# Performance work log

Hardware: AMD Instinct MI355X
Metric: run time of the kernel (lower is better)

The kernel has to match this reference:

```python
import jax, jax.numpy as jnp
import numpy as np

B, S, HID, NH, NS = 2, 1024, 2048, 16, 8
D = HID // NH  # head_dim = 128


def setup_inputs() -> dict:
    key = jax.random.key(0)
    ks = jax.random.split(key, 8)
    inv = 1.0 / np.sqrt(HID)
    return {
        "hidden_states": jax.random.normal(ks[0], (B, S, HID), jnp.float32),
        "Wq": jax.random.normal(ks[1], (HID, HID), jnp.float32) * inv,
        "Wk": jax.random.normal(ks[2], (HID, HID), jnp.float32) * inv,
        "Wv": jax.random.normal(ks[3], (HID, HID), jnp.float32) * inv,
        "Wo": jax.random.normal(ks[4], (HID, HID), jnp.float32) * inv,
        "splat_positions": jax.random.normal(ks[5], (NH, NS, D), jnp.float32) * 0.02,
        "splat_directions": jax.random.normal(ks[6], (NH, NS, D), jnp.float32) * 0.02,
        "splat_log_scales": jnp.full((NH, NS), np.log(0.8), jnp.float32),
        "splat_log_amplitudes": jnp.full((NH, NS), -np.log(float(NS)), jnp.float32),
        "directional_strength": jnp.float32(0.3),
        "gsa_strength": jnp.float32(-6.0),
    }


def _affinities(tokens, positions, directions, scales, dir_strength):
    # tokens [B,NH,S,D]; positions/directions [NH,NS,D]; scales [NH,NS]
    tok_sq = jnp.sum(tokens * tokens, axis=-1)                       # [B,NH,S]
    pos_sq = jnp.sum(positions * positions, axis=-1)                 # [NH,NS]
    tp = jnp.einsum('bhsd,hnd->bhsn', tokens, positions)             # [B,NH,S,NS]
    dist2 = tok_sq[..., None] - 2.0 * tp + pos_sq[None, :, None, :]
    dist2 = jnp.maximum(dist2, 0.0)
    # signed projection of (token - position) onto unit direction
    proj = (jnp.einsum('bhsd,hnd->bhsn', tokens, directions)
            - jnp.sum(positions * directions, axis=-1)[None, :, None, :])
    perp2 = jnp.maximum(dist2 - proj * proj, 0.0)
    inv2s2 = (0.5 / (scales * scales))[None, :, None, :]
    radial = jnp.exp(-dist2 * inv2s2)
    directional = jnp.exp(-perp2 * inv2s2)
    return (1.0 - dir_strength) * radial + dir_strength * directional


def reference(hidden_states, Wq, Wk, Wv, Wo, splat_positions, splat_directions,
              splat_log_scales, splat_log_amplitudes, directional_strength, gsa_strength):
    b, s, hid = hidden_states.shape

    def heads(x):  # [B,S,HID] -> [B,NH,S,D]
        return x.reshape(b, s, NH, D).transpose(0, 2, 1, 3)

    q = heads(hidden_states @ Wq)
    k = heads(hidden_states @ Wk)
    v = heads(hidden_states @ Wv)

    # --- standard (original) attention path ---
    scores = jnp.einsum('bhqd,bhkd->bhqk', q, k) / jnp.sqrt(jnp.float32(D))
    attn = jax.nn.softmax(scores, axis=-1)
    std = jnp.einsum('bhqk,bhkd->bhqd', attn, v)
    std = std.transpose(0, 2, 1, 3).reshape(b, s, hid) @ Wo

    # --- directional GSA path ---
    eps = 1e-12
    positions = splat_positions / (jnp.linalg.norm(splat_positions, axis=-1, keepdims=True) + eps)
    positions = positions * (np.sqrt(D) * 0.3)
    directions = splat_directions / (jnp.linalg.norm(splat_directions, axis=-1, keepdims=True) + eps)
    scales = jnp.clip(jnp.exp(splat_log_scales), 0.3, 1.2)
    amplitudes = jax.nn.softmax(splat_log_amplitudes, axis=-1)
    ds = jax.nn.sigmoid(directional_strength)

    qa = _affinities(q, positions, directions, scales, ds)  # [B,NH,S,NS]
    ka = _affinities(k, positions, directions, scales, ds)  # [B,NH,S,NS]
    w = jnp.einsum('bhqn,hn,bhkn->bhqk', qa, amplitudes, ka)
    w = w / (jnp.sum(w, axis=-1, keepdims=True) + 1e-8)
    dgsa = jnp.einsum('bhqk,bhkd->bhqd', w, v)
    dgsa = dgsa.transpose(0, 2, 1, 3).reshape(b, s, hid) @ Wo

    gsa = jax.nn.sigmoid(gsa_strength)
    blend = jnp.minimum(0.05, gsa * 0.1)
    return (1.0 - blend) * std + blend * dgsa
```

## Files before the change

### kernel.cpp

```cpp
#include <hip/hip_runtime.h>
#include <math.h>

typedef __attribute__((ext_vector_type(8))) short bf16x8;
typedef __attribute__((ext_vector_type(4))) float f32x4;
typedef unsigned short ushort_t;

__device__ __forceinline__ unsigned short f2b(float f) {
    unsigned u = __float_as_uint(f);
    unsigned r = (u + 0x7fffu + ((u >> 16) & 1u)) >> 16;
    return (unsigned short)r;
}
__device__ __forceinline__ float b2f(unsigned short h) {
    return __uint_as_float(((unsigned)h) << 16);
}

__device__ __forceinline__ void async_copy16(const void* g, void* l) {
    __builtin_amdgcn_global_load_lds((const __attribute__((address_space(1))) void*)g,
                                     (__attribute__((address_space(3))) void*)l, 16, 0, 0);
}

__global__ void splat_prep(const float* __restrict__ sp, const float* __restrict__ sd,
                           const float* __restrict__ ls, const float* __restrict__ la,
                           float* __restrict__ posn, float* __restrict__ dirn,
                           float* __restrict__ pos_sq, float* __restrict__ pdv,
                           float* __restrict__ iv2s2, float* __restrict__ amp) {
    int i = threadIdx.x;
    const float* p = sp + (size_t)i * 128;
    const float* d = sd + (size_t)i * 128;
    float np_ = 0.f, nd_ = 0.f;
    for (int k = 0; k < 128; ++k) { np_ += p[k] * p[k]; nd_ += d[k] * d[k]; }
    np_ = sqrtf(np_); nd_ = sqrtf(nd_);
    const float sc = 3.394112549695428f;
    float rp = sc / (np_ + 1e-12f);
    float rd = 1.f / (nd_ + 1e-12f);
    float psq = 0.f, pd_ = 0.f;
    for (int k = 0; k < 128; ++k) {
        float pn = p[k] * rp;
        float dn = d[k] * rd;
        posn[(size_t)i * 128 + k] = pn;
        dirn[(size_t)i * 128 + k] = dn;
        psq += pn * pn;
        pd_ += pn * dn;
    }
    pos_sq[i] = psq;
    pdv[i] = pd_;
    float s = expf(ls[i]);
    s = fminf(fmaxf(s, 0.3f), 1.2f);
    iv2s2[i] = 0.5f / (s * s);
    if ((i & 7) == 0) {
        int h = i >> 3;
        float mx = -INFINITY;
        for (int n = 0; n < 8; ++n) mx = fmaxf(mx, la[h * 8 + n]);
        float e[8]; float ssum = 0.f;
        for (int n = 0; n < 8; ++n) { e[n] = expf(la[h * 8 + n] - mx); ssum += e[n]; }
        for (int n = 0; n < 8; ++n) amp[h * 8 + n] = e[n] / ssum;
    }
}

__global__ __launch_bounds__(256) void convert_x(const float* __restrict__ X,
                                                 ushort_t* __restrict__ Y) {
    int i = (blockIdx.x * 256 + threadIdx.x) * 4;
    float4 v = *(const float4*)(X + i);
    ushort4 o;
    o.x = f2b(v.x); o.y = f2b(v.y); o.z = f2b(v.z); o.w = f2b(v.w);
    *(ushort4*)(Y + i) = o;
}

__global__ __launch_bounds__(256) void transpose_all(const float* __restrict__ W0,
                                                     const float* __restrict__ W1,
                                                     const float* __restrict__ W2,
                                                     const float* __restrict__ W3,
                                                     ushort_t* __restrict__ WT4) {
    __shared__ float t[32][33];
    int z = blockIdx.z;
    const float* W = (z == 0) ? W0 : (z == 1) ? W1 : (z == 2) ? W2 : W3;
    ushort_t* WT = WT4 + (size_t)z * 4194304;
    int tx = threadIdx.x & 31, ty = threadIdx.x >> 5;
    int bn = blockIdx.x * 32, bk = blockIdx.y * 32;
#pragma unroll
    for (int i = 0; i < 4; ++i)
        t[ty + i * 8][tx] = W[(size_t)(bk + ty + i * 8) * 2048 + bn + tx];
    __syncthreads();
#pragma unroll
    for (int i = 0; i < 4; ++i)
        WT[(size_t)(bn + ty + i * 8) * 2048 + bk + tx] = f2b(t[tx][ty + i * 8]);
}


__global__ __launch_bounds__(256) void gemm_qkv(const ushort_t* __restrict__ A,
                                                const ushort_t* __restrict__ WT4,
                                                ushort_t* __restrict__ Qb,
                                                ushort_t* __restrict__ Kb,
                                                ushort_t* __restrict__ Vb,
                                                ushort_t* __restrict__ Vt) {
    __shared__ ushort_t As[128 * 32];
    __shared__ ushort_t Bs[128 * 32];
    const int tid = threadIdx.x, lane = tid & 63, wave = tid >> 6;
    const int l15 = lane & 15, quad = lane >> 4;
    const int wm = (wave >> 1) * 64, wn = (wave & 1) * 64;
    const int bm = blockIdx.x * 128;
    const int by = blockIdx.y, which = by >> 4, bn = (by & 15) * 128;
    const ushort_t* BT = WT4 + (size_t)which * 4194304;
    f32x4 acc[4][4] = {};
    const int off0 = tid * 16;
    const int row0 = tid >> 2;
    const int c0 = (tid & 3) ^ ((row0 + (row0 >> 2)) & 3);
    const ushort_t* ga = A + (size_t)(bm + row0) * 2048 + c0 * 8;
    const ushort_t* gb = BT + (size_t)(bn + row0) * 2048 + c0 * 8;
    const int rsw = (l15 + (l15 >> 2)) & 3;
    for (int k0 = 0; k0 < 2048; k0 += 32) {
        __syncthreads();
        async_copy16(ga + k0, (char*)As + off0);
        async_copy16(ga + (size_t)64 * 2048 + k0, (char*)As + off0 + 4096);
        async_copy16(gb + k0, (char*)Bs + off0);
        async_copy16(gb + (size_t)64 * 2048 + k0, (char*)Bs + off0 + 4096);
        __syncthreads();
        bf16x8 af[4], bfr[4];
#pragma unroll
        for (int i = 0; i < 4; ++i)
            af[i] = *(const bf16x8*)((const char*)As + (wm + i * 16 + l15) * 64 + ((quad ^ rsw) << 4));
#pragma unroll
        for (int j = 0; j < 4; ++j)
            bfr[j] = *(const bf16x8*)((const char*)Bs + (wn + j * 16 + l15) * 64 + ((quad ^ rsw) << 4));
#pragma unroll
        for (int i = 0; i < 4; ++i)
#pragma unroll
            for (int j = 0; j < 4; ++j)
                acc[i][j] = __builtin_amdgcn_mfma_f32_16x16x32_bf16(af[i], bfr[j], acc[i][j], 0, 0, 0);
    }
    ushort_t* Cb = (which == 0) ? Qb : ((which == 1) ? Kb : Vb);
    const bool dot = (which == 2);
    const float oscale = (which == 0) ? 0.08838834764831845f : 1.f;
#pragma unroll
    for (int i = 0; i < 4; ++i) {
#pragma unroll
        for (int j = 0; j < 4; ++j) {
            int m0 = bm + wm + i * 16 + quad * 4;
            int n = bn + wn + j * 16 + l15;
            int b = m0 >> 10, s0 = m0 & 1023, h = n >> 7, d = n & 127;
            ushort4 pack;
            unsigned short* pp = (unsigned short*)&pack;
#pragma unroll
            for (int r = 0; r < 4; ++r) {
                unsigned short bv = f2b(acc[i][j][r] * oscale);
                pp[r] = bv;
                Cb[((size_t)((b << 4) | h) * 1024 + (s0 + r)) * 128 + d] = bv;
            }
            if (dot) *(ushort4*)(Vt + ((size_t)((b << 4) | h) * 128 + d) * 1024 + s0) = pack;
        }
    }
}

__global__ __launch_bounds__(256) void gemm_out(const ushort_t* __restrict__ A,
                                                const ushort_t* __restrict__ BT,
                                                float* __restrict__ Cf) {
    __shared__ ushort_t As[128 * 32];
    __shared__ ushort_t Bs[64 * 32];
    const int tid = threadIdx.x, lane = tid & 63, wave = tid >> 6;
    const int l15 = lane & 15, quad = lane >> 4;
    const int wm = (wave >> 1) * 64, wn = (wave & 1) * 32;
    const int bm = blockIdx.x * 128, bn = blockIdx.y * 64;
    f32x4 acc[4][2] = {};
    const int off0 = tid * 16;
    const int row0 = tid >> 2;
    const int c0 = (tid & 3) ^ ((row0 + (row0 >> 2)) & 3);
    const ushort_t* ga = A + (size_t)(bm + row0) * 2048 + c0 * 8;
    const ushort_t* gb = BT + (size_t)(bn + row0) * 2048 + c0 * 8;
    const int rsw = (l15 + (l15 >> 2)) & 3;
    for (int k0 = 0; k0 < 2048; k0 += 32) {
        __syncthreads();
        async_copy16(ga + k0, (char*)As + off0);
        async_copy16(ga + (size_t)64 * 2048 + k0, (char*)As + off0 + 4096);
        async_copy16(gb + k0, (char*)Bs + off0);
        __syncthreads();
        bf16x8 af[4], bfr[2];
#pragma unroll
        for (int i = 0; i < 4; ++i)
            af[i] = *(const bf16x8*)((const char*)As + (wm + i * 16 + l15) * 64 + ((quad ^ rsw) << 4));
#pragma unroll
        for (int j = 0; j < 2; ++j)
            bfr[j] = *(const bf16x8*)((const char*)Bs + (wn + j * 16 + l15) * 64 + ((quad ^ rsw) << 4));
#pragma unroll
        for (int i = 0; i < 4; ++i)
#pragma unroll
            for (int j = 0; j < 2; ++j)
                acc[i][j] = __builtin_amdgcn_mfma_f32_16x16x32_bf16(af[i], bfr[j], acc[i][j], 0, 0, 0);
    }
#pragma unroll
    for (int i = 0; i < 4; ++i)
#pragma unroll
        for (int j = 0; j < 2; ++j)
#pragma unroll
            for (int r = 0; r < 4; ++r) {
                int m = bm + wm + i * 16 + quad * 4 + r;
                int n = bn + wn + j * 16 + l15;
                Cf[(size_t)m * 2048 + n] = acc[i][j][r];
            }
}

__global__ __launch_bounds__(256) void affinity_kernel(
    const ushort_t* __restrict__ Q, const ushort_t* __restrict__ K,
    const float* __restrict__ posn, const float* __restrict__ dirn,
    const float* __restrict__ pos_sq, const float* __restrict__ pdv,
    const float* __restrict__ iv2s2, const float* __restrict__ ds_in,
    float* __restrict__ qa, float* __restrict__ ka) {
    int gid = blockIdx.x * 256 + threadIdx.x;
    int n = gid & 7;
    int t = (gid >> 3) & 32767;
    int which = gid >> 18;
    const ushort_t* T = (which ? K : Q) + (size_t)t * 128;
    int h = (t >> 10) & 15;
    const float* P = posn + (size_t)(h * 8 + n) * 128;
    const float* Dr = dirn + (size_t)(h * 8 + n) * 128;
    float tsq = 0.f, tp = 0.f, td = 0.f;
#pragma unroll
    for (int d = 0; d < 128; d += 8) {
        uint4 raw = *(const uint4*)(T + d);
        float tv[8];
        tv[0] = __uint_as_float(raw.x << 16); tv[1] = __uint_as_float(raw.x & 0xffff0000u);
        tv[2] = __uint_as_float(raw.y << 16); tv[3] = __uint_as_float(raw.y & 0xffff0000u);
        tv[4] = __uint_as_float(raw.z << 16); tv[5] = __uint_as_float(raw.z & 0xffff0000u);
        tv[6] = __uint_as_float(raw.w << 16); tv[7] = __uint_as_float(raw.w & 0xffff0000u);
        float4 p0 = *(const float4*)(P + d), p1 = *(const float4*)(P + d + 4);
        float4 d0 = *(const float4*)(Dr + d), d1 = *(const float4*)(Dr + d + 4);
        tsq += tv[0]*tv[0]+tv[1]*tv[1]+tv[2]*tv[2]+tv[3]*tv[3]+tv[4]*tv[4]+tv[5]*tv[5]+tv[6]*tv[6]+tv[7]*tv[7];
        tp  += tv[0]*p0.x+tv[1]*p0.y+tv[2]*p0.z+tv[3]*p0.w+tv[4]*p1.x+tv[5]*p1.y+tv[6]*p1.z+tv[7]*p1.w;
        td  += tv[0]*d0.x+tv[1]*d0.y+tv[2]*d0.z+tv[3]*d0.w+tv[4]*d1.x+tv[5]*d1.y+tv[6]*d1.z+tv[7]*d1.w;
    }
    float fs = which ? 1.f : 11.313708498984761f;
    tsq *= fs * fs; tp *= fs; td *= fs;
    float dist2 = fmaxf(tsq - 2.f * tp + pos_sq[h * 8 + n], 0.f);
    float proj = td - pdv[h * 8 + n];
    float perp2 = fmaxf(dist2 - proj * proj, 0.f);
    float iv = iv2s2[h * 8 + n];
    float dsv = 1.f / (1.f + __expf(-ds_in[0]));
    float aff = (1.f - dsv) * __expf(-dist2 * iv) + dsv * __expf(-perp2 * iv);
    (which ? ka : qa)[(size_t)t * 8 + n] = aff;
}

__global__ __launch_bounds__(128) void kv_s1_part(const float* __restrict__ ka,
                                                  const ushort_t* __restrict__ V,
                                                  float* __restrict__ KVp,
                                                  float* __restrict__ S1p) {
    int bh = blockIdx.x, sc = blockIdx.y;
    int d = threadIdx.x;
    const float* kaB = ka + ((size_t)bh * 1024 + sc * 128) * 8;
    const ushort_t* VB = V + ((size_t)bh * 1024 + sc * 128) * 128;
    float acc[8] = {};
#pragma unroll 4
    for (int s = 0; s < 128; ++s) {
        float vd = b2f(VB[(size_t)s * 128 + d]);
        float4 k0 = *(const float4*)(kaB + (size_t)s * 8);
        float4 k1 = *(const float4*)(kaB + (size_t)s * 8 + 4);
        acc[0] += k0.x * vd; acc[1] += k0.y * vd; acc[2] += k0.z * vd; acc[3] += k0.w * vd;
        acc[4] += k1.x * vd; acc[5] += k1.y * vd; acc[6] += k1.z * vd; acc[7] += k1.w * vd;
    }
#pragma unroll
    for (int n = 0; n < 8; ++n) KVp[(((size_t)bh * 8 + n) * 8 + sc) * 128 + d] = acc[n];
    __shared__ float s1p[128];
    {
        int n = d >> 4, chunk = d & 15;
        float p = 0.f;
        for (int s = chunk * 8; s < chunk * 8 + 8; ++s) p += kaB[(size_t)s * 8 + n];
        s1p[d] = p;
    }
    __syncthreads();
    if (d < 8) {
        float t = 0.f;
        for (int c = 0; c < 16; ++c) t += s1p[(d << 4) + c];
        S1p[((size_t)bh * 8 + d) * 8 + sc] = t;
    }
}

__global__ __launch_bounds__(256) void flash_blend(
    const ushort_t* __restrict__ Qg, const ushort_t* __restrict__ Kg,
    const ushort_t* __restrict__ Vtg,
    const float* __restrict__ qa, const float* __restrict__ amp,
    const float* __restrict__ S1p, const float* __restrict__ KVp,
    const float* __restrict__ gstr, ushort_t* __restrict__ blended) {
    __shared__ ushort_t Ks[2][64 * 128];
    __shared__ ushort_t Vt[2][128 * 64];
    __shared__ ushort_t Ps[4][16 * 72];
    __shared__ float KVs[8 * 128];
    __shared__ float S1s[8];
    const int tid = threadIdx.x, lane = tid & 63, wave = tid >> 6;
    const int l15 = lane & 15, quad = lane >> 4;
    const int bh = blockIdx.y, qt = blockIdx.x;

    const ushort_t* Qrow = Qg + ((size_t)(bh * 1024 + qt * 64 + wave * 16 + l15)) * 128 + quad * 8;
    bf16x8 aq[4];
#pragma unroll
    for (int k4 = 0; k4 < 4; ++k4) aq[k4] = *(const bf16x8*)(Qrow + k4 * 32);

    {
        int n = tid >> 5, d = (tid & 31) * 4;
        f32x4 kv = {};
#pragma unroll
        for (int sc = 0; sc < 8; ++sc)
            kv += *(const f32x4*)(KVp + (((size_t)bh * 8 + n) * 8 + sc) * 128 + d);
        *(f32x4*)(KVs + tid * 4) = kv;
    }
    if (tid < 8) {
        float s = 0.f;
#pragma unroll
        for (int sc = 0; sc < 8; ++sc) s += S1p[((size_t)bh * 8 + tid) * 8 + sc];
        S1s[tid] = s;
    }

    const ushort_t* Kbase = Kg + (size_t)bh * 131072;
    const ushort_t* Vbase = Vtg + (size_t)bh * 131072;

#define STAGE(buf, kt_)                                                               \
    {                                                                                 \
        _Pragma("unroll") for (int i_ = 0; i_ < 4; ++i_) {                            \
            int off_ = tid * 16 + i_ * 4096;                                          \
            int kr_ = off_ >> 8, kp_ = (off_ >> 4) & 15;                              \
            async_copy16(Kbase + (size_t)(kt_)*8192 + kr_ * 128 + ((kp_ ^ (kr_ & 15)) << 3), \
                         (char*)(&Ks[buf][0]) + off_);                                \
            int vd_ = off_ >> 7, vp_ = (off_ >> 4) & 7;                               \
            async_copy16(Vbase + (size_t)vd_ * 1024 + (kt_)*64 + ((vp_ ^ (vd_ & 7)) << 3), \
                         (char*)(&Vt[buf][0]) + off_);                                \
        }                                                                             \
    }

    STAGE(0, 0);

    f32x4 o[8] = {};
    float l_i[4] = {};
    ushort_t* Pw = &Ps[wave][0];

    for (int kt = 0; kt < 16; ++kt) {
        __syncthreads();
        if (kt < 15) STAGE((kt + 1) & 1, kt + 1);
        const int cb = kt & 1;
        f32x4 sc[4] = {};
#pragma unroll
        for (int k4 = 0; k4 < 4; ++k4) {
#pragma unroll
            for (int t = 0; t < 4; ++t) {
                bf16x8 bk = *(const bf16x8*)((const char*)&Ks[cb][0] +
                                             ((t * 16 + l15) << 8) + (((k4 * 4 + quad) ^ l15) << 4));
                sc[t] = __builtin_amdgcn_mfma_f32_16x16x32_bf16(aq[k4], bk, sc[t], 0, 0, 0);
            }
        }
#pragma unroll
        for (int t = 0; t < 4; ++t) {
#pragma unroll
            for (int r = 0; r < 4; ++r) {
                float p = __expf(sc[t][r]);
                l_i[r] += p;
                Pw[(quad * 4 + r) * 72 + t * 16 + l15] = f2b(p);
            }
        }
        bf16x8 ap0 = *(const bf16x8*)((const char*)Pw + (l15 * 72 + quad * 8) * 2);
        bf16x8 ap1 = *(const bf16x8*)((const char*)Pw + (l15 * 72 + 32 + quad * 8) * 2);
#pragma unroll
        for (int j = 0; j < 8; ++j) {
            bf16x8 bv0 = *(const bf16x8*)((const char*)&Vt[cb][0] +
                                          ((j * 16 + l15) << 7) + (((quad) ^ (l15 & 7)) << 4));
            bf16x8 bv1 = *(const bf16x8*)((const char*)&Vt[cb][0] +
                                          ((j * 16 + l15) << 7) + (((4 + quad) ^ (l15 & 7)) << 4));
            o[j] = __builtin_amdgcn_mfma_f32_16x16x32_bf16(ap0, bv0, o[j], 0, 0, 0);
            o[j] = __builtin_amdgcn_mfma_f32_16x16x32_bf16(ap1, bv1, o[j], 0, 0, 0);
        }
    }
#undef STAGE
#pragma unroll
    for (int r = 0; r < 4; ++r) {
        float l = l_i[r];
        l += __shfl_xor(l, 1);
        l += __shfl_xor(l, 2);
        l += __shfl_xor(l, 4);
        l += __shfl_xor(l, 8);
        l_i[r] = l;
    }
    float gsa = 1.f / (1.f + __expf(-gstr[0]));
    float blend = fminf(0.05f, gsa * 0.1f);
    int b = bh >> 4, h = bh & 15;
#pragma unroll
    for (int r = 0; r < 4; ++r) {
        int q = qt * 64 + wave * 16 + quad * 4 + r;
        const float* qaRow = qa + ((size_t)bh * 1024 + q) * 8;
        float qam[8], Z = 0.f;
#pragma unroll
        for (int n = 0; n < 8; ++n) {
            qam[n] = qaRow[n] * amp[h * 8 + n];
            Z += qam[n] * S1s[n];
        }
        float invZ = 1.f / (Z + 1e-8f);
        float invl = 1.f / l_i[r];
        ushort_t* outp = blended + ((size_t)(b * 1024 + q)) * 2048 + h * 128;
#pragma unroll
        for (int j = 0; j < 8; ++j) {
            int d = j * 16 + l15;
            float dg = 0.f;
#pragma unroll
            for (int n = 0; n < 8; ++n) dg += qam[n] * KVs[n * 128 + d];
            float v = (1.f - blend) * (o[j][r] * invl) + blend * (dg * invZ);
            outp[d] = f2b(v);
        }
    }
}

extern "C" void kernel_launch(void* const* d_in, const int* in_sizes, int n_in,
                              void* d_out, int out_size, void* d_ws, size_t ws_size,
                              hipStream_t stream) {
    const float* X = (const float*)d_in[0];
    const float* Wq = (const float*)d_in[1];
    const float* Wk = (const float*)d_in[2];
    const float* Wv = (const float*)d_in[3];
    const float* Wo = (const float*)d_in[4];
    const float* sp = (const float*)d_in[5];
    const float* sd = (const float*)d_in[6];
    const float* ls = (const float*)d_in[7];
    const float* la = (const float*)d_in[8];
    const float* dstr = (const float*)d_in[9];
    const float* gstr = (const float*)d_in[10];

    char* base = (char*)d_ws;
    ushort_t* WT4 = (ushort_t*)base;      base += 33554432;
    ushort_t* Xbf = (ushort_t*)base;      base += 8388608;
    ushort_t* blended = Xbf;
    ushort_t* Qbf = (ushort_t*)base;      base += 8388608;
    ushort_t* Kbf = (ushort_t*)base;      base += 8388608;
    ushort_t* Vbf = (ushort_t*)base;      base += 8388608;
    ushort_t* Vtb = (ushort_t*)base;      base += 8388608;
    float* qaw = (float*)base;            base += 1048576;
    float* kaw = (float*)base;            base += 1048576;
    float* posn = (float*)base;           base += 65536;
    float* dirn = (float*)base;           base += 65536;
    float* pos_sq = (float*)base;         base += 512;
    float* pdv = (float*)base;            base += 512;
    float* iv2s2 = (float*)base;          base += 512;
    float* ampw = (float*)base;           base += 512;
    float* S1p = (float*)base;            base += 8192;
    float* KVp = (float*)base;            base += 1048576;

    splat_prep<<<1, 128, 0, stream>>>(sp, sd, ls, la, posn, dirn, pos_sq, pdv, iv2s2, ampw);
    convert_x<<<4096, 256, 0, stream>>>(X, Xbf);
    transpose_all<<<dim3(64, 64, 4), 256, 0, stream>>>(Wq, Wk, Wv, Wo, WT4);

    gemm_qkv<<<dim3(16, 48), 256, 0, stream>>>(Xbf, WT4, Qbf, Kbf, Vbf, Vtb);

    affinity_kernel<<<2048, 256, 0, stream>>>(Qbf, Kbf, posn, dirn, pos_sq, pdv, iv2s2, dstr, qaw, kaw);
    kv_s1_part<<<dim3(32, 8), 128, 0, stream>>>(kaw, Vbf, KVp, S1p);

    flash_blend<<<dim3(16, 32), 256, 0, stream>>>(Qbf, Kbf, Vtb, qaw, ampw, S1p, KVp, gstr, blended);
    gemm_out<<<dim3(16, 32), 256, 0, stream>>>(blended, WT4 + 12582912, (float*)d_out);
}
```

Measured before the change: 366.3 us.

## Merge prep kernels, double-buffer GEMM smem, fuse query affinities into flash kernel

Folds splat prep, X conversion and the weight transposes into one launch so fewer kernels are dispatched. Both GEMMs gain a second shared-memory buffer so the next K tile's async load overlaps the current MFMA work and one barrier per step is dropped. Query affinities are now computed inside flash_blend from the Q fragments already in registers, which removes the qa buffer and halves the affinity kernel. The risks are higher LDS use in the GEMMs, which may lower occupancy, and serial per-thread dot products against posn/dirn inside the attention kernel. The double-buffer loop no longer waits for the async copies to finish before reading LDS, which may be a correctness hazard.

```diff
diff --git a/kernel.cpp b/kernel.cpp
--- a/kernel.cpp
+++ b/kernel.cpp
@@ -4,6 +4,9 @@
 typedef __attribute__((ext_vector_type(8))) short bf16x8;
 typedef __attribute__((ext_vector_type(4))) float f32x4;
 typedef unsigned short ushort_t;
+
+#define SQRT_D 11.313708498984761f
+#define INV_SQRT_D 0.08838834764831845f
 
 __device__ __forceinline__ unsigned short f2b(float f) {
     unsigned u = __float_as_uint(f);
@@ -19,71 +22,73 @@
                                      (__attribute__((address_space(3))) void*)l, 16, 0, 0);
 }
 
-__global__ void splat_prep(const float* __restrict__ sp, const float* __restrict__ sd,
-                           const float* __restrict__ ls, const float* __restrict__ la,
-                           float* __restrict__ posn, float* __restrict__ dirn,
-                           float* __restrict__ pos_sq, float* __restrict__ pdv,
-                           float* __restrict__ iv2s2, float* __restrict__ amp) {
-    int i = threadIdx.x;
-    const float* p = sp + (size_t)i * 128;
-    const float* d = sd + (size_t)i * 128;
-    float np_ = 0.f, nd_ = 0.f;
-    for (int k = 0; k < 128; ++k) { np_ += p[k] * p[k]; nd_ += d[k] * d[k]; }
-    np_ = sqrtf(np_); nd_ = sqrtf(nd_);
-    const float sc = 3.394112549695428f;
-    float rp = sc / (np_ + 1e-12f);
-    float rd = 1.f / (nd_ + 1e-12f);
-    float psq = 0.f, pd_ = 0.f;
-    for (int k = 0; k < 128; ++k) {
-        float pn = p[k] * rp;
-        float dn = d[k] * rd;
-        posn[(size_t)i * 128 + k] = pn;
-        dirn[(size_t)i * 128 + k] = dn;
-        psq += pn * pn;
-        pd_ += pn * dn;
-    }
-    pos_sq[i] = psq;
-    pdv[i] = pd_;
-    float s = expf(ls[i]);
-    s = fminf(fmaxf(s, 0.3f), 1.2f);
-    iv2s2[i] = 0.5f / (s * s);
-    if ((i & 7) == 0) {
-        int h = i >> 3;
-        float mx = -INFINITY;
-        for (int n = 0; n < 8; ++n) mx = fmaxf(mx, la[h * 8 + n]);
-        float e[8]; float ssum = 0.f;
-        for (int n = 0; n < 8; ++n) { e[n] = expf(la[h * 8 + n] - mx); ssum += e[n]; }
-        for (int n = 0; n < 8; ++n) amp[h * 8 + n] = e[n] / ssum;
-    }
-}
-
-__global__ __launch_bounds__(256) void convert_x(const float* __restrict__ X,
-                                                 ushort_t* __restrict__ Y) {
-    int i = (blockIdx.x * 256 + threadIdx.x) * 4;
-    float4 v = *(const float4*)(X + i);
-    ushort4 o;
-    o.x = f2b(v.x); o.y = f2b(v.y); o.z = f2b(v.z); o.w = f2b(v.w);
-    *(ushort4*)(Y + i) = o;
-}
-
-__global__ __launch_bounds__(256) void transpose_all(const float* __restrict__ W0,
-                                                     const float* __restrict__ W1,
-                                                     const float* __restrict__ W2,
-                                                     const float* __restrict__ W3,
-                                                     ushort_t* __restrict__ WT4) {
+__global__ __launch_bounds__(256) void prep(
+    const float* __restrict__ X, const float* __restrict__ W0,
+    const float* __restrict__ W1, const float* __restrict__ W2,
+    const float* __restrict__ W3, const float* __restrict__ sp,
+    const float* __restrict__ sd, const float* __restrict__ ls,
+    const float* __restrict__ la, ushort_t* __restrict__ Xbf,
+    ushort_t* __restrict__ WT4, float* __restrict__ posn,
+    float* __restrict__ dirn, float* __restrict__ pos_sq,
+    float* __restrict__ pdv, float* __restrict__ iv2s2,
+    float* __restrict__ amp) {
     __shared__ float t[32][33];
-    int z = blockIdx.z;
-    const float* W = (z == 0) ? W0 : (z == 1) ? W1 : (z == 2) ? W2 : W3;
-    ushort_t* WT = WT4 + (size_t)z * 4194304;
-    int tx = threadIdx.x & 31, ty = threadIdx.x >> 5;
-    int bn = blockIdx.x * 32, bk = blockIdx.y * 32;
-#pragma unroll
-    for (int i = 0; i < 4; ++i)
-        t[ty + i * 8][tx] = W[(size_t)(bk + ty + i * 8) * 2048 + bn + tx];
-    __syncthreads();
-#pragma unroll
-    for (int i = 0; i < 4; ++i)
-        WT[(size_t)(bn + ty + i * 8) * 2048 + bk + tx] = f2b(t[tx][ty + i * 8]);
+    const int z = blockIdx.z;
+    if (z < 4) {
+        const float* W = (z == 0) ? W0 : (z == 1) ? W1 : (z == 2) ? W2 : W3;
+        ushort_t* WT = WT4 + (size_t)z * 4194304;
+        int tx = threadIdx.x & 31, ty = threadIdx.x >> 5;
+        int bn = blockIdx.x * 32, bk = blockIdx.y * 32;
+#pragma unroll
+        for (int i = 0; i < 4; ++i)
+            t[ty + i * 8][tx] = W[(size_t)(bk + ty + i * 8) * 2048 + bn + tx];
+        __syncthreads();
+#pragma unroll
+        for (int i = 0; i < 4; ++i)
+            WT[(size_t)(bn + ty + i * 8) * 2048 + bk + tx] = f2b(t[tx][ty + i * 8]);
+        return;
+    }
+    {
+        int bi = blockIdx.y * 64 + blockIdx.x;
+        int i = (bi * 256 + threadIdx.x) * 4;
+        float4 v = *(const float4*)(X + i);
+        ushort4 o;
+        o.x = f2b(v.x); o.y = f2b(v.y); o.z = f2b(v.z); o.w = f2b(v.w);
+        *(ushort4*)(Xbf + i) = o;
+    }
+    if (blockIdx.x == 0 && blockIdx.y == 0 && threadIdx.x < 128) {
+        int i = threadIdx.x;
+        const float* p = sp + (size_t)i * 128;
+        const float* d = sd + (size_t)i * 128;
+        float np_ = 0.f, nd_ = 0.f;
+        for (int k = 0; k < 128; ++k) { np_ += p[k] * p[k]; nd_ += d[k] * d[k]; }
+        np_ = sqrtf(np_); nd_ = sqrtf(nd_);
+        const float sc = 3.394112549695428f;
+        float rp = sc / (np_ + 1e-12f);
+        float rd = 1.f / (nd_ + 1e-12f);
+        float psq = 0.f, pd_ = 0.f;
+        for (int k = 0; k < 128; ++k) {
+            float pn = p[k] * rp;
+            float dn = d[k] * rd;
+            posn[(size_t)i * 128 + k] = pn;
+            dirn[(size_t)i * 128 + k] = dn;
+            psq += pn * pn;
+            pd_ += pn * dn;
+        }
+        pos_sq[i] = psq;
+        pdv[i] = pd_;
+        float s = expf(ls[i]);
+        s = fminf(fmaxf(s, 0.3f), 1.2f);
+        iv2s2[i] = 0.5f / (s * s);
+        if ((i & 7) == 0) {
+            int h = i >> 3;
+            float mx = -INFINITY;
+            for (int n = 0; n < 8; ++n) mx = fmaxf(mx, la[h * 8 + n]);
+            float e[8]; float ssum = 0.f;
+            for (int n = 0; n < 8; ++n) { e[n] = expf(la[h * 8 + n] - mx); ssum += e[n]; }
+            for (int n = 0; n < 8; ++n) amp[h * 8 + n] = e[n] / ssum;
+        }
+    }
 }
 
 
@@ -93,8 +98,8 @@
                                                 ushort_t* __restrict__ Kb,
                                                 ushort_t* __restrict__ Vb,
                                                 ushort_t* __restrict__ Vt) {
-    __shared__ ushort_t As[128 * 32];
-    __shared__ ushort_t Bs[128 * 32];
+    __shared__ ushort_t As[2][128 * 32];
+    __shared__ ushort_t Bs[2][128 * 32];
     const int tid = threadIdx.x, lane = tid & 63, wave = tid >> 6;
     const int l15 = lane & 15, quad = lane >> 4;
     const int wm = (wave >> 1) * 64, wn = (wave & 1) * 64;
@@ -108,29 +113,35 @@
     const ushort_t* ga = A + (size_t)(bm + row0) * 2048 + c0 * 8;
     const ushort_t* gb = BT + (size_t)(bn + row0) * 2048 + c0 * 8;
     const int rsw = (l15 + (l15 >> 2)) & 3;
+#define STAGEG(buf_, k_)                                                      \
+    {                                                                         \
+        async_copy16(ga + (k_), (char*)As[buf_] + off0);                      \
+        async_copy16(ga + (size_t)64 * 2048 + (k_), (char*)As[buf_] + off0 + 4096); \
+        async_copy16(gb + (k_), (char*)Bs[buf_] + off0);                      \
+        async_copy16(gb + (size_t)64 * 2048 + (k_), (char*)Bs[buf_] + off0 + 4096); \
+    }
+    STAGEG(0, 0);
     for (int k0 = 0; k0 < 2048; k0 += 32) {
         __syncthreads();
-        async_copy16(ga + k0, (char*)As + off0);
-        async_copy16(ga + (size_t)64 * 2048 + k0, (char*)As + off0 + 4096);
-        async_copy16(gb + k0, (char*)Bs + off0);
-        async_copy16(gb + (size_t)64 * 2048 + k0, (char*)Bs + off0 + 4096);
-        __syncthreads();
+        if (k0 < 2016) STAGEG(((k0 >> 5) + 1) & 1, k0 + 32);
+        const int cb = (k0 >> 5) & 1;
         bf16x8 af[4], bfr[4];
 #pragma unroll
         for (int i = 0; i < 4; ++i)
-            af[i] = *(const bf16x8*)((const char*)As + (wm + i * 16 + l15) * 64 + ((quad ^ rsw) << 4));
+            af[i] = *(const bf16x8*)((const char*)As[cb] + (wm + i * 16 + l15) * 64 + ((quad ^ rsw) << 4));
 #pragma unroll
         for (int j = 0; j < 4; ++j)
-            bfr[j] = *(const bf16x8*)((const char*)Bs + (wn + j * 16 + l15) * 64 + ((quad ^ rsw) << 4));
+            bfr[j] = *(const bf16x8*)((const char*)Bs[cb] + (wn + j * 16 + l15) * 64 + ((quad ^ rsw) << 4));
 #pragma unroll
         for (int i = 0; i < 4; ++i)
 #pragma unroll
             for (int j = 0; j < 4; ++j)
                 acc[i][j] = __builtin_amdgcn_mfma_f32_16x16x32_bf16(af[i], bfr[j], acc[i][j], 0, 0, 0);
     }
+#undef STAGEG
     ushort_t* Cb = (which == 0) ? Qb : ((which == 1) ? Kb : Vb);
     const bool dot = (which == 2);
-    const float oscale = (which == 0) ? 0.08838834764831845f : 1.f;
+    const float oscale = (which == 0) ? INV_SQRT_D : 1.f;
 #pragma unroll
     for (int i = 0; i < 4; ++i) {
 #pragma unroll
@@ -154,8 +165,8 @@
 __global__ __launch_bounds__(256) void gemm_out(const ushort_t* __restrict__ A,
                                                 const ushort_t* __restrict__ BT,
                                                 float* __restrict__ Cf) {
-    __shared__ ushort_t As[128 * 32];
-    __shared__ ushort_t Bs[64 * 32];
+    __shared__ ushort_t As[2][128 * 32];
+    __shared__ ushort_t Bs[2][64 * 32];
     const int tid = threadIdx.x, lane = tid & 63, wave = tid >> 6;
     const int l15 = lane & 15, quad = lane >> 4;
     const int wm = (wave >> 1) * 64, wn = (wave & 1) * 32;
@@ -167,25 +178,31 @@
     const ushort_t* ga = A + (size_t)(bm + row0) * 2048 + c0 * 8;
     const ushort_t* gb = BT + (size_t)(bn + row0) * 2048 + c0 * 8;
     const int rsw = (l15 + (l15 >> 2)) & 3;
+#define STAGEO(buf_, k_)                                                      \
+    {                                                                         \
+        async_copy16(ga + (k_), (char*)As[buf_] + off0);                      \
+        async_copy16(ga + (size_t)64 * 2048 + (k_), (char*)As[buf_] + off0 + 4096); \
+        async_copy16(gb + (k_), (char*)Bs[buf_] + off0);                      \
+    }
+    STAGEO(0, 0);
     for (int k0 = 0; k0 < 2048; k0 += 32) {
         __syncthreads();
-        async_copy16(ga + k0, (char*)As + off0);
-        async_copy16(ga + (size_t)64 * 2048 + k0, (char*)As + off0 + 4096);
-        async_copy16(gb + k0, (char*)Bs + off0);
-        __syncthreads();
+        if (k0 < 2016) STAGEO(((k0 >> 5) + 1) & 1, k0 + 32);
+        const int cb = (k0 >> 5) & 1;
         bf16x8 af[4], bfr[2];
 #pragma unroll
         for (int i = 0; i < 4; ++i)
-            af[i] = *(const bf16x8*)((const char*)As + (wm + i * 16 + l15) * 64 + ((quad ^ rsw) << 4));
+            af[i] = *(const bf16x8*)((const char*)As[cb] + (wm + i * 16 + l15) * 64 + ((quad ^ rsw) << 4));
 #pragma unroll
         for (int j = 0; j < 2; ++j)
-            bfr[j] = *(const bf16x8*)((const char*)Bs + (wn + j * 16 + l15) * 64 + ((quad ^ rsw) << 4));
+            bfr[j] = *(const bf16x8*)((const char*)Bs[cb] + (wn + j * 16 + l15) * 64 + ((quad ^ rsw) << 4));
 #pragma unroll
         for (int i = 0; i < 4; ++i)
 #pragma unroll
             for (int j = 0; j < 2; ++j)
                 acc[i][j] = __builtin_amdgcn_mfma_f32_16x16x32_bf16(af[i], bfr[j], acc[i][j], 0, 0, 0);
     }
+#undef STAGEO
 #pragma unroll
     for (int i = 0; i < 4; ++i)
 #pragma unroll
@@ -198,17 +215,16 @@
             }
 }
 
-__global__ __launch_bounds__(256) void affinity_kernel(
-    const ushort_t* __restrict__ Q, const ushort_t* __restrict__ K,
+__global__ __launch_bounds__(256) void affinity_k(
+    const ushort_t* __restrict__ K,
     const float* __restrict__ posn, const float* __restrict__ dirn,
     const float* __restrict__ pos_sq, const float* __restrict__ pdv,
     const float* __restrict__ iv2s2, const float* __restrict__ ds_in,
-    float* __restrict__ qa, float* __restrict__ ka) {
+    float* __restrict__ ka) {
     int gid = blockIdx.x * 256 + threadIdx.x;
     int n = gid & 7;
-    int t = (gid >> 3) & 32767;
-    int which = gid >> 18;
-    const ushort_t* T = (which ? K : Q) + (size_t)t * 128;
+    int t = gid >> 3;
+    const ushort_t* T = K + (size_t)t * 128;
     int h = (t >> 10) & 15;
     const float* P = posn + (size_t)(h * 8 + n) * 128;
     const float* Dr = dirn + (size_t)(h * 8 + n) * 128;
@@ -227,15 +243,13 @@
         tp  += tv[0]*p0.x+tv[1]*p0.y+tv[2]*p0.z+tv[3]*p0.w+tv[4]*p1.x+tv[5]*p1.y+tv[6]*p1.z+tv[7]*p1.w;
         td  += tv[0]*d0.x+tv[1]*d0.y+tv[2]*d0.z+tv[3]*d0.w+tv[4]*d1.x+tv[5]*d1.y+tv[6]*d1.z+tv[7]*d1.w;
     }
-    float fs = which ? 1.f : 11.313708498984761f;
-    tsq *= fs * fs; tp *= fs; td *= fs;
     float dist2 = fmaxf(tsq - 2.f * tp + pos_sq[h * 8 + n], 0.f);
     float proj = td - pdv[h * 8 + n];
     float perp2 = fmaxf(dist2 - proj * proj, 0.f);
     float iv = iv2s2[h * 8 + n];
     float dsv = 1.f / (1.f + __expf(-ds_in[0]));
     float aff = (1.f - dsv) * __expf(-dist2 * iv) + dsv * __expf(-perp2 * iv);
-    (which ? ka : qa)[(size_t)t * 8 + n] = aff;
+    ka[(size_t)t * 8 + n] = aff;
 }
 
 __global__ __launch_bounds__(128) void kv_s1_part(const float* __restrict__ ka,
@@ -275,7 +289,10 @@
 __global__ __launch_bounds__(256) void flash_blend(
     const ushort_t* __restrict__ Qg, const ushort_t* __restrict__ Kg,
     const ushort_t* __restrict__ Vtg,
-    const float* __restrict__ qa, const float* __restrict__ amp,
+    const float* __restrict__ posn, const float* __restrict__ dirn,
+    const float* __restrict__ pos_sq, const float* __restrict__ pdv,
+    const float* __restrict__ iv2s2, const float* __restrict__ ds_in,
+    const float* __restrict__ amp,
     const float* __restrict__ S1p, const float* __restrict__ KVp,
     const float* __restrict__ gstr, ushort_t* __restrict__ blended) {
     __shared__ ushort_t Ks[2][64 * 128];
@@ -283,14 +300,47 @@
     __shared__ ushort_t Ps[4][16 * 72];
     __shared__ float KVs[8 * 128];
     __shared__ float S1s[8];
+    __shared__ float qas[4][16][8];
     const int tid = threadIdx.x, lane = tid & 63, wave = tid >> 6;
     const int l15 = lane & 15, quad = lane >> 4;
     const int bh = blockIdx.y, qt = blockIdx.x;
+    const int h = bh & 15;
 
     const ushort_t* Qrow = Qg + ((size_t)(bh * 1024 + qt * 64 + wave * 16 + l15)) * 128 + quad * 8;
     bf16x8 aq[4];
 #pragma unroll
     for (int k4 = 0; k4 < 4; ++k4) aq[k4] = *(const bf16x8*)(Qrow + k4 * 32);
+
+    {
+        float tsq = 0.f, tp[8] = {}, td[8] = {};
+#pragma unroll
+        for (int k4 = 0; k4 < 4; ++k4) {
+#pragma unroll
+            for (int j = 0; j < 8; ++j) {
+                float qv = b2f((unsigned short)aq[k4][j]) * SQRT_D;
+                int d = k4 * 32 + quad * 8 + j;
+                tsq += qv * qv;
+#pragma unroll
+                for (int n = 0; n < 8; ++n) {
+                    tp[n] += qv * posn[(size_t)(h * 8 + n) * 128 + d];
+                    td[n] += qv * dirn[(size_t)(h * 8 + n) * 128 + d];
+                }
+            }
+        }
+        tsq += __shfl_xor(tsq, 16); tsq += __shfl_xor(tsq, 32);
+        float dsv = 1.f / (1.f + __expf(-ds_in[0]));
+#pragma unroll
+        for (int n = 0; n < 8; ++n) {
+            float a = tp[n]; a += __shfl_xor(a, 16); a += __shfl_xor(a, 32);
+            float bb = td[n]; bb += __shfl_xor(bb, 16); bb += __shfl_xor(bb, 32);
+            float dist2 = fmaxf(tsq - 2.f * a + pos_sq[h * 8 + n], 0.f);
+            float proj = bb - pdv[h * 8 + n];
+            float perp2 = fmaxf(dist2 - proj * proj, 0.f);
+            float iv = iv2s2[h * 8 + n];
+            float aff = (1.f - dsv) * __expf(-dist2 * iv) + dsv * __expf(-perp2 * iv);
+            if (quad == 0) qas[wave][l15][n] = aff;
+        }
+    }
 
     {
         int n = tid >> 5, d = (tid & 31) * 4;
@@ -376,15 +426,14 @@
     }
     float gsa = 1.f / (1.f + __expf(-gstr[0]));
     float blend = fminf(0.05f, gsa * 0.1f);
-    int b = bh >> 4, h = bh & 15;
+    int b = bh >> 4;
 #pragma unroll
     for (int r = 0; r < 4; ++r) {
         int q = qt * 64 + wave * 16 + quad * 4 + r;
-        const float* qaRow = qa + ((size_t)bh * 1024 + q) * 8;
         float qam[8], Z = 0.f;
 #pragma unroll
         for (int n = 0; n < 8; ++n) {
-            qam[n] = qaRow[n] * amp[h * 8 + n];
+            qam[n] = qas[wave][quad * 4 + r][n] * amp[h * 8 + n];
             Z += qam[n] * S1s[n];
         }
         float invZ = 1.f / (Z + 1e-8f);
@@ -425,7 +474,6 @@
     ushort_t* Kbf = (ushort_t*)base;      base += 8388608;
     ushort_t* Vbf = (ushort_t*)base;      base += 8388608;
     ushort_t* Vtb = (ushort_t*)base;      base += 8388608;
-    float* qaw = (float*)base;            base += 1048576;
     float* kaw = (float*)base;            base += 1048576;
     float* posn = (float*)base;           base += 65536;
     float* dirn = (float*)base;           base += 65536;
@@ -436,15 +484,12 @@
     float* S1p = (float*)base;            base += 8192;
     float* KVp = (float*)base;            base += 1048576;
 
-    splat_prep<<<1, 128, 0, stream>>>(sp, sd, ls, la, posn, dirn, pos_sq, pdv, iv2s2, ampw);
-    convert_x<<<4096, 256, 0, stream>>>(X, Xbf);
-    transpose_all<<<dim3(64, 64, 4), 256, 0, stream>>>(Wq, Wk, Wv, Wo, WT4);
-
+    prep<<<dim3(64, 64, 5), 256, 0, stream>>>(X, Wq, Wk, Wv, Wo, sp, sd, ls, la,
+                                              Xbf, WT4, posn, dirn, pos_sq, pdv, iv2s2, ampw);
     gemm_qkv<<<dim3(16, 48), 256, 0, stream>>>(Xbf, WT4, Qbf, Kbf, Vbf, Vtb);
-
-    affinity_kernel<<<2048, 256, 0, stream>>>(Qbf, Kbf, posn, dirn, pos_sq, pdv, iv2s2, dstr, qaw, kaw);
+    affinity_k<<<1024, 256, 0, stream>>>(Kbf, posn, dirn, pos_sq, pdv, iv2s2, dstr, kaw);
     kv_s1_part<<<dim3(32, 8), 128, 0, stream>>>(kaw, Vbf, KVp, S1p);
-
-    flash_blend<<<dim3(16, 32), 256, 0, stream>>>(Qbf, Kbf, Vtb, qaw, ampw, S1p, KVp, gstr, blended);
+    flash_blend<<<dim3(16, 32), 256, 0, stream>>>(Qbf, Kbf, Vtb, posn, dirn, pos_sq, pdv,
+                                                  iv2s2, dstr, ampw, S1p, KVp, gstr, blended);
     gemm_out<<<dim3(16, 32), 256, 0, stream>>>(blended, WT4 + 12582912, (float*)d_out);
 }
```

Result: slower. 374.1 us (+2.1%).
